# Performance work log

Hardware: AMD Instinct MI355X
Metric: run time of the kernel (lower is better)

The kernel has to match this reference:

```python
import jax, jax.numpy as jnp
import numpy as np

N_ATOMS = 100000
N_EDGES = 200000  # paired: edge 2i and 2i+1 are reverses of each other
N_MOLS = 4096
D_V, D_E, D_H = 133, 14, 512
DEPTH = 3
BN_EPS = 1e-5


def setup_inputs() -> dict:
    key = jax.random.key(0)
    ks = jax.random.split(key, 10)
    V = jax.random.normal(ks[0], (N_ATOMS, D_V), dtype=jnp.float32)
    E = jax.random.normal(ks[1], (N_EDGES, D_E), dtype=jnp.float32)
    # paired directed edges: (src,dst) at 2i, (dst,src) at 2i+1 -> rev index is i^1
    half = N_EDGES // 2
    s = jax.random.randint(ks[2], (half,), 0, N_ATOMS, dtype=jnp.int32)
    d = jax.random.randint(ks[3], (half,), 0, N_ATOMS, dtype=jnp.int32)
    edge_src = jnp.stack([s, d], axis=1).reshape(-1)
    edge_dst = jnp.stack([d, s], axis=1).reshape(-1)
    batch = jnp.sort(jax.random.randint(ks[4], (N_ATOMS,), 0, N_MOLS, dtype=jnp.int32))
    sc = 0.02
    W_i = jax.random.normal(ks[5], (D_V + D_E, D_H), dtype=jnp.float32) * sc
    W_h = jax.random.normal(ks[6], (D_H, D_H), dtype=jnp.float32) * sc
    W_o = jax.random.normal(ks[7], (D_V + D_H, D_H), dtype=jnp.float32) * sc
    b_o = jnp.zeros((D_H,), dtype=jnp.float32)
    gamma = jnp.ones((D_H,), dtype=jnp.float32)
    beta = jnp.zeros((D_H,), dtype=jnp.float32)
    return {"V": V, "E": E, "edge_src": edge_src, "edge_dst": edge_dst,
            "batch": batch, "W_i": W_i, "W_h": W_h, "W_o": W_o, "b_o": b_o,
            "gamma": gamma, "beta": beta}


def reference(V, E, edge_src, edge_dst, batch, W_i, W_h, W_o, b_o, gamma, beta):
    n_atoms = V.shape[0]
    n_edges = E.shape[0]
    rev = jnp.arange(n_edges, dtype=jnp.int32) ^ 1  # reverse-bond index

    # --- BondMessagePassing (chemprop v2) ---
    # initialize: H_0 = W_i([V[src] ; E]), H = relu(H_0)
    H0 = jnp.concatenate([V[edge_src], E], axis=1) @ W_i  # [n_edges, d_h]
    H = jax.nn.relu(H0)
    for _ in range(DEPTH - 1):
        # message: sum of incoming edge states at dst node, gathered at src,
        # minus the reverse edge's own state
        M_node = jax.ops.segment_sum(H, edge_dst, num_segments=n_atoms)
        M = M_node[edge_src] - H[rev]
        # update: H = relu(H_0 + W_h(M)) (dropout = 0)
        H = jax.nn.relu(H0 + M @ W_h)
    # finalize: aggregate edges to nodes, H_v = relu(W_o([V ; M_v]))
    M_v = jax.ops.segment_sum(H, edge_dst, num_segments=n_atoms)
    H_v = jax.nn.relu(jnp.concatenate([V, M_v], axis=1) @ W_o + b_o)  # [n_atoms, d_h]

    # --- MeanAggregation over batch ids ---
    sums = jax.ops.segment_sum(H_v, batch, num_segments=N_MOLS)
    counts = jax.ops.segment_sum(jnp.ones((n_atoms,), H_v.dtype), batch, num_segments=N_MOLS)
    h_mol = sums / jnp.maximum(counts, 1.0)[:, None]  # [n_mols, d_h]

    # --- BatchNorm1d (training mode: batch statistics, biased variance) ---
    mu = h_mol.mean(axis=0)
    var = h_mol.var(axis=0)
    return (h_mol - mu) * jax.lax.rsqrt(var + BN_EPS) * gamma + beta
```

## Files before the change

### kernel.cpp

```cpp
#include <hip/hip_runtime.h>

typedef _Float16 f16;
typedef _Float16 half8 __attribute__((ext_vector_type(8)));
typedef _Float16 half4v __attribute__((ext_vector_type(4)));
typedef float f32x4 __attribute__((ext_vector_type(4)));

#define N_ATOMS 100000
#define N_EDGES 200000
#define N_MOLS  4096
#define D_V 133
#define D_E 14
#define D_H 512
#define KC  672
#define KSE 21
#define LDA 40

__global__ void wt_build_swz(const float* __restrict__ W1, int r1,
                             const float* __restrict__ W2, int r2,
                             f16* __restrict__ WtS) {
    int gid = blockIdx.x * blockDim.x + threadIdx.x;
    if (gid >= D_H * KC) return;
    int n = gid / KC;
    int k = gid - n * KC;
    float x = 0.f;
    if (k < r1) x = W1[k * D_H + n];
    else if (k < r1 + r2) x = W2[(k - r1) * D_H + n];
    const int dst = ((((n >> 4) * KSE + (k >> 5)) << 6) + (((k >> 3) & 3) << 4) + (n & 15)) * 8 + (k & 7);
    WtS[dst] = (f16)x;
}

__global__ void csr_hist(const int* __restrict__ edst, int* __restrict__ cnt) {
    int e = blockIdx.x * blockDim.x + threadIdx.x;
    if (e < N_EDGES) atomicAdd(&cnt[edst[e]], 1);
}

__global__ __launch_bounds__(1024) void csr_scan(const int* __restrict__ cnt,
                                                 int* __restrict__ off, int* __restrict__ pos) {
    __shared__ int sums[1024];
    const int tid = threadIdx.x;
    const int lo = tid * 98;
    const int hi = min(lo + 98, N_ATOMS);
    int s = 0;
    for (int i = lo; i < hi; ++i) s += cnt[i];
    sums[tid] = s;
    __syncthreads();
    for (int d = 1; d < 1024; d <<= 1) {
        int v = (tid >= d) ? sums[tid - d] : 0;
        __syncthreads();
        sums[tid] += v;
        __syncthreads();
    }
    int run = sums[tid] - s;
    for (int i = lo; i < hi; ++i) { off[i] = run; pos[i] = run; run += cnt[i]; }
    if (tid == 1023) off[N_ATOMS] = run;
}

__global__ void csr_scatter(const int* __restrict__ edst, int* __restrict__ pos,
                            int* __restrict__ eid) {
    int e = blockIdx.x * blockDim.x + threadIdx.x;
    if (e < N_EDGES) {
        int idx = atomicAdd(&pos[edst[e]], 1);
        eid[idx] = e;
    }
}

__global__ __launch_bounds__(512) void seg_csr(
    const f16* __restrict__ H, const int* __restrict__ off, const int* __restrict__ eid,
    unsigned int* __restrict__ MnQ32, float* __restrict__ Msc)
{
    const int n = blockIdx.x * 8 + (threadIdx.x >> 6);
    const int lane = threadIdx.x & 63;
    const int j0 = off[n], j1 = off[n + 1];
    float acc[8];
    #pragma unroll
    for (int k = 0; k < 8; ++k) acc[k] = 0.f;
    for (int j = j0; j < j1; ++j) {
        const int e = eid[j];
        const half8 h = *reinterpret_cast<const half8*>(&H[e * D_H + lane * 8]);
        #pragma unroll
        for (int k = 0; k < 8; ++k) acc[k] += (float)h[k];
    }
    float m = 0.f;
    #pragma unroll
    for (int k = 0; k < 8; ++k) m = fmaxf(m, fabsf(acc[k]));
    m = fmaxf(m, __shfl_xor(m, 1));
    m = fmaxf(m, __shfl_xor(m, 2));
    m = fmaxf(m, 1e-20f);
    const float s = m * (1.f / 127.f);
    const float inv_s = 127.f / m;
    if ((lane & 3) == 0) Msc[n * 16 + (lane >> 2)] = s;
    int q[8];
    #pragma unroll
    for (int k = 0; k < 8; ++k) q[k] = __float2int_rn(acc[k] * inv_s);
    uint2 o;
    o.x = (q[0] & 0xff) | ((q[1] & 0xff) << 8) | ((q[2] & 0xff) << 16) | ((unsigned)(q[3] & 0xff) << 24);
    o.y = (q[4] & 0xff) | ((q[5] & 0xff) << 8) | ((q[6] & 0xff) << 16) | ((unsigned)(q[7] & 0xff) << 24);
    *reinterpret_cast<uint2*>(&MnQ32[n * 128 + lane * 2]) = o;
}

__global__ __launch_bounds__(512) void gemm_pass(
    const float* __restrict__ V, const float* __restrict__ E,
    const int* __restrict__ esrc, const char* __restrict__ MnQ,
    const float* __restrict__ Msc,
    f16* __restrict__ Ha, const f16* __restrict__ WtS, int ks_begin)
{
    __shared__ __align__(16) f16 Al[64 * LDA];
    const int tid = threadIdx.x;
    const int rowblk = blockIdx.x << 6;
    const int srow = tid >> 3;
    const int skk  = (tid & 7) << 2;
    const int e_s  = rowblk + srow;
    const int sv   = esrc[e_s];
    const int rev  = e_s ^ 1;
    const int lane = tid & 63;
    const int quad = lane >> 4;
    const int m16  = lane & 15;
    const int colbase = (tid >> 6) << 6;
    const int cb0 = (tid >> 6) << 2;
    const f16* WtL = WtS + lane * 8;

    f32x4 acc[4][4];
    #pragma unroll
    for (int a = 0; a < 4; ++a)
    #pragma unroll
    for (int b = 0; b < 4; ++b)
    #pragma unroll
    for (int r = 0; r < 4; ++r) acc[a][b][r] = 0.f;

    char4 pq; float ps; half4v ph; float pv[4];
    auto issue = [&](int ks) {
        const int k0 = ks << 5;
        if (k0 < D_H) {
            pq = *reinterpret_cast<const char4*>(&MnQ[sv * D_H + k0 + skk]);
            ps = Msc[sv * 16 + (k0 >> 5)];
            ph = *reinterpret_cast<const half4v*>(&Ha[rev * D_H + k0 + skk]);
        } else {
            #pragma unroll
            for (int j = 0; j < 4; ++j) {
                const int kk = k0 + skk + j - D_H;
                float x = 0.f;
                if (kk < D_V) x = V[sv * D_V + kk];
                else if (kk < D_V + D_E) x = E[e_s * D_E + (kk - D_V)];
                pv[j] = x;
            }
        }
    };

    issue(ks_begin);
    for (int ks = ks_begin; ks < KSE; ++ks) {
        const int k0 = ks << 5;
        half4v w;
        if (k0 < D_H) {
            w[0] = (f16)((float)pq.x * ps - (float)ph[0]);
            w[1] = (f16)((float)pq.y * ps - (float)ph[1]);
            w[2] = (f16)((float)pq.z * ps - (float)ph[2]);
            w[3] = (f16)((float)pq.w * ps - (float)ph[3]);
        } else {
            w[0] = (f16)pv[0]; w[1] = (f16)pv[1]; w[2] = (f16)pv[2]; w[3] = (f16)pv[3];
        }
        __syncthreads();
        *reinterpret_cast<half4v*>(&Al[srow * LDA + skk]) = w;
        __syncthreads();
        if (ks + 1 < KSE) issue(ks + 1);
        half8 af[4];
        #pragma unroll
        for (int rt = 0; rt < 4; ++rt)
            af[rt] = *reinterpret_cast<const half8*>(&Al[(rt * 16 + m16) * LDA + quad * 8]);
        #pragma unroll
        for (int ct = 0; ct < 4; ++ct) {
            const half8 bf = *reinterpret_cast<const half8*>(&WtL[(((cb0 + ct) * KSE + ks) << 9)]);
            #pragma unroll
            for (int rt = 0; rt < 4; ++rt)
                acc[rt][ct] = __builtin_amdgcn_mfma_f32_16x16x32_f16(af[rt], bf, acc[rt][ct], 0, 0, 0);
        }
    }

    #pragma unroll
    for (int rt = 0; rt < 4; ++rt)
    #pragma unroll
    for (int ct = 0; ct < 4; ++ct)
    #pragma unroll
    for (int r = 0; r < 4; ++r) {
        const int row = rowblk + rt * 16 + quad * 4 + r;
        const int col = colbase + ct * 16 + m16;
        Ha[row * D_H + col] = (f16)fmaxf(acc[rt][ct][r], 0.f);
    }
}

__global__ __launch_bounds__(512) void gemm_out(
    const float* __restrict__ V, const char* __restrict__ MnQ,
    const float* __restrict__ Msc, const float* __restrict__ bo,
    const f16* __restrict__ WtS, f16* __restrict__ Hv)
{
    __shared__ __align__(16) f16 Al[64 * LDA];
    __shared__ float bo_s[D_H];
    const int tid = threadIdx.x;
    const int rowblk = blockIdx.x << 6;
    bo_s[tid] = bo[tid];
    const int srow = tid >> 3;
    const int skk  = (tid & 7) << 2;
    const int arow = min(rowblk + srow, N_ATOMS - 1);
    const int lane = tid & 63;
    const int quad = lane >> 4;
    const int m16  = lane & 15;
    const int colbase = (tid >> 6) << 6;
    const int cb0 = (tid >> 6) << 2;
    const f16* WtL = WtS + lane * 8;

    f32x4 acc[4][4];
    #pragma unroll
    for (int a = 0; a < 4; ++a)
    #pragma unroll
    for (int b = 0; b < 4; ++b)
    #pragma unroll
    for (int r = 0; r < 4; ++r) acc[a][b][r] = 0.f;

    char4 pq; float ps; float pv[4];
    auto issue = [&](int ks) {
        const int k0 = ks << 5;
        if (k0 < D_H) {
            pq = *reinterpret_cast<const char4*>(&MnQ[arow * D_H + k0 + skk]);
            ps = Msc[arow * 16 + (k0 >> 5)];
        } else {
            #pragma unroll
            for (int j = 0; j < 4; ++j) {
                const int kk = k0 + skk + j - D_H;
                pv[j] = (kk < D_V) ? V[arow * D_V + kk] : 0.f;
            }
        }
    };

    issue(0);
    for (int ks = 0; ks < KSE; ++ks) {
        const int k0 = ks << 5;
        half4v w;
        if (k0 < D_H) {
            w[0] = (f16)((float)pq.x * ps);
            w[1] = (f16)((float)pq.y * ps);
            w[2] = (f16)((float)pq.z * ps);
            w[3] = (f16)((float)pq.w * ps);
        } else {
            w[0] = (f16)pv[0]; w[1] = (f16)pv[1]; w[2] = (f16)pv[2]; w[3] = (f16)pv[3];
        }
        __syncthreads();
        *reinterpret_cast<half4v*>(&Al[srow * LDA + skk]) = w;
        __syncthreads();
        if (ks + 1 < KSE) issue(ks + 1);
        half8 af[4];
        #pragma unroll
        for (int rt = 0; rt < 4; ++rt)
            af[rt] = *reinterpret_cast<const half8*>(&Al[(rt * 16 + m16) * LDA + quad * 8]);
        #pragma unroll
        for (int ct = 0; ct < 4; ++ct) {
            const half8 bf = *reinterpret_cast<const half8*>(&WtL[(((cb0 + ct) * KSE + ks) << 9)]);
            #pragma unroll
            for (int rt = 0; rt < 4; ++rt)
                acc[rt][ct] = __builtin_amdgcn_mfma_f32_16x16x32_f16(af[rt], bf, acc[rt][ct], 0, 0, 0);
        }
    }

    #pragma unroll
    for (int rt = 0; rt < 4; ++rt)
    #pragma unroll
    for (int ct = 0; ct < 4; ++ct)
    #pragma unroll
    for (int r = 0; r < 4; ++r) {
        const int row = rowblk + rt * 16 + quad * 4 + r;
        if (row < N_ATOMS) {
            const int col = colbase + ct * 16 + m16;
            Hv[row * D_H + col] = (f16)fmaxf(acc[rt][ct][r] + bo_s[col], 0.f);
        }
    }
}

__global__ __launch_bounds__(512) void mol_mean(
    const f16* __restrict__ Hv, const int* __restrict__ batch, float* __restrict__ mean)
{
    const int m = blockIdx.x;
    __shared__ int sh[2];
    if (threadIdx.x == 0) {
        int lo = 0, hi = N_ATOMS;
        while (lo < hi) { int mid = (lo + hi) >> 1; if (batch[mid] < m) lo = mid + 1; else hi = mid; }
        sh[0] = lo;
        int lo2 = lo; hi = N_ATOMS;
        while (lo2 < hi) { int mid = (lo2 + hi) >> 1; if (batch[mid] < m + 1) lo2 = mid + 1; else hi = mid; }
        sh[1] = lo2;
    }
    __syncthreads();
    const int a0 = sh[0], a1 = sh[1];
    float acc = 0.f;
    for (int a = a0; a < a1; ++a) acc += (float)Hv[(size_t)a * D_H + threadIdx.x];
    mean[m * D_H + threadIdx.x] = acc / (float)max(a1 - a0, 1);
}

__global__ __launch_bounds__(256) void bn_stats(
    const float* __restrict__ mean_in, const float* __restrict__ gamma,
    const float* __restrict__ beta, float* __restrict__ An, float* __restrict__ Bn)
{
    const int n = blockIdx.x;
    const int tid = threadIdx.x;
    float s = 0.f, s2 = 0.f;
    for (int m = tid; m < N_MOLS; m += 256) {
        float h = mean_in[m * D_H + n];
        s += h; s2 += h * h;
    }
    for (int off = 32; off > 0; off >>= 1) {
        s  += __shfl_down(s, off);
        s2 += __shfl_down(s2, off);
    }
    __shared__ float sh[8];
    const int wave = tid >> 6, lane = tid & 63;
    if (lane == 0) { sh[wave] = s; sh[4 + wave] = s2; }
    __syncthreads();
    if (tid == 0) {
        float S  = sh[0] + sh[1] + sh[2] + sh[3];
        float S2 = sh[4] + sh[5] + sh[6] + sh[7];
        float mu = S / (float)N_MOLS;
        float var = fmaxf(S2 / (float)N_MOLS - mu * mu, 0.f);
        float sc = rsqrtf(var + 1e-5f) * gamma[n];
        An[n] = sc;
        Bn[n] = beta[n] - mu * sc;
    }
}

__global__ void bn_apply(const float* __restrict__ mean_in,
                         const float* __restrict__ An, const float* __restrict__ Bn,
                         float* __restrict__ out)
{
    int gid = blockIdx.x * blockDim.x + threadIdx.x;
    int n = gid & 511;
    out[gid] = mean_in[gid] * An[n] + Bn[n];
}

extern "C" void kernel_launch(void* const* d_in, const int* in_sizes, int n_in,
                              void* d_out, int out_size, void* d_ws, size_t ws_size,
                              hipStream_t stream)
{
    (void)in_sizes; (void)n_in; (void)out_size; (void)ws_size;
    const float* V     = (const float*)d_in[0];
    const float* E     = (const float*)d_in[1];
    const int*   esrc  = (const int*)d_in[2];
    const int*   edst  = (const int*)d_in[3];
    const int*   batch = (const int*)d_in[4];
    const float* Wi    = (const float*)d_in[5];
    const float* Wh    = (const float*)d_in[6];
    const float* Wo    = (const float*)d_in[7];
    const float* bo    = (const float*)d_in[8];
    const float* gam   = (const float*)d_in[9];
    const float* bet   = (const float*)d_in[10];
    float* out = (float*)d_out;

    char* ws = (char*)d_ws;
    f16*   WtC  = (f16*)(ws + 0);
    f16*   WtO  = (f16*)(ws + 688128);
    int*   off  = (int*)(ws + 1376256);
    int*   eid  = (int*)(ws + 1776384);
    int*   cnt  = (int*)(ws + 2576384);
    float* An   = (float*)(ws + 2992768);
    float* Bn   = (float*)(ws + 2994816);
    f16*   Ha   = (f16*)(ws + 2996864);
    char*  MnQ  = (char*)(ws + 207796864);
    float* Msc  = (float*)(ws + 258996864);
    unsigned int* MnQ32 = (unsigned int*)MnQ;
    f16*   Hv   = Ha;
    float* mean = out;

    wt_build_swz<<<(D_H * KC + 255) / 256, 256, 0, stream>>>(Wh, D_H, Wi, D_V + D_E, WtC);
    wt_build_swz<<<(D_H * KC + 255) / 256, 256, 0, stream>>>(Wo + D_V * D_H, D_H, Wo, D_V, WtO);

    hipMemsetAsync(cnt, 0, 400000, stream);
    csr_hist<<<(N_EDGES + 511) / 512, 512, 0, stream>>>(edst, cnt);
    csr_scan<<<1, 1024, 0, stream>>>(cnt, off, cnt);
    csr_scatter<<<(N_EDGES + 511) / 512, 512, 0, stream>>>(edst, cnt, eid);

    gemm_pass<<<N_EDGES / 64, 512, 0, stream>>>(V, E, esrc, MnQ, Msc, Ha, WtC, 16);

    for (int it = 0; it < 2; ++it) {
        seg_csr<<<N_ATOMS / 8, 512, 0, stream>>>(Ha, off, eid, MnQ32, Msc);
        gemm_pass<<<N_EDGES / 64, 512, 0, stream>>>(V, E, esrc, MnQ, Msc, Ha, WtC, 0);
    }

    seg_csr<<<N_ATOMS / 8, 512, 0, stream>>>(Ha, off, eid, MnQ32, Msc);

    gemm_out<<<(N_ATOMS + 63) / 64, 512, 0, stream>>>(V, MnQ, Msc, bo, WtO, Hv);
    mol_mean<<<N_MOLS, 512, 0, stream>>>(Hv, batch, mean);
    bn_stats<<<D_H, 256, 0, stream>>>(mean, gam, bet, An, Bn);
    bn_apply<<<(N_MOLS * D_H) / 256, 256, 0, stream>>>(mean, An, Bn, out);
}
```

Before: 1.516 ms.

## Retile GEMM blocks to 32 rows by 4 waves and dequantize in fp16

Both GEMM kernels move from 64-row tiles with 8 waves to 32-row tiles with 4 waves, each wave covering 128 output columns (2x8 MFMA tiles instead of 4x4). The aim is more blocks, smaller LDS tiles and possibly better occupancy. The cost is that each B fragment from global or L2 is now shared by only 2 row tiles instead of 4, which roughly doubles weight traffic per output. Separately, the int8 message dequantization now runs in packed fp16 arithmetic instead of fp32, trading a little precision for fewer conversion instructions.

```diff
diff --git a/kernel.cpp b/kernel.cpp
--- a/kernel.cpp
+++ b/kernel.cpp
@@ -98,15 +98,15 @@
     *reinterpret_cast<uint2*>(&MnQ32[n * 128 + lane * 2]) = o;
 }
 
-__global__ __launch_bounds__(512) void gemm_pass(
+__global__ __launch_bounds__(256) void gemm_pass(
     const float* __restrict__ V, const float* __restrict__ E,
     const int* __restrict__ esrc, const char* __restrict__ MnQ,
     const float* __restrict__ Msc,
     f16* __restrict__ Ha, const f16* __restrict__ WtS, int ks_begin)
 {
-    __shared__ __align__(16) f16 Al[64 * LDA];
+    __shared__ __align__(16) f16 Al[32 * LDA];
     const int tid = threadIdx.x;
-    const int rowblk = blockIdx.x << 6;
+    const int rowblk = blockIdx.x << 5;
     const int srow = tid >> 3;
     const int skk  = (tid & 7) << 2;
     const int e_s  = rowblk + srow;
@@ -115,24 +115,24 @@
     const int lane = tid & 63;
     const int quad = lane >> 4;
     const int m16  = lane & 15;
-    const int colbase = (tid >> 6) << 6;
-    const int cb0 = (tid >> 6) << 2;
+    const int colbase = (tid >> 6) << 7;
+    const int cb0 = (tid >> 6) << 3;
     const f16* WtL = WtS + lane * 8;
 
-    f32x4 acc[4][4];
-    #pragma unroll
-    for (int a = 0; a < 4; ++a)
-    #pragma unroll
-    for (int b = 0; b < 4; ++b)
+    f32x4 acc[2][8];
+    #pragma unroll
+    for (int a = 0; a < 2; ++a)
+    #pragma unroll
+    for (int b = 0; b < 8; ++b)
     #pragma unroll
     for (int r = 0; r < 4; ++r) acc[a][b][r] = 0.f;
 
-    char4 pq; float ps; half4v ph; float pv[4];
+    char4 pq; f16 psh; half4v ph; float pv[4];
     auto issue = [&](int ks) {
         const int k0 = ks << 5;
         if (k0 < D_H) {
             pq = *reinterpret_cast<const char4*>(&MnQ[sv * D_H + k0 + skk]);
-            ps = Msc[sv * 16 + (k0 >> 5)];
+            psh = (f16)Msc[sv * 16 + (k0 >> 5)];
             ph = *reinterpret_cast<const half4v*>(&Ha[rev * D_H + k0 + skk]);
         } else {
             #pragma unroll
@@ -148,13 +148,15 @@
 
     issue(ks_begin);
     for (int ks = ks_begin; ks < KSE; ++ks) {
-        const int k0 = ks << 5;
         half4v w;
-        if (k0 < D_H) {
-            w[0] = (f16)((float)pq.x * ps - (float)ph[0]);
-            w[1] = (f16)((float)pq.y * ps - (float)ph[1]);
-            w[2] = (f16)((float)pq.z * ps - (float)ph[2]);
-            w[3] = (f16)((float)pq.w * ps - (float)ph[3]);
+        if ((ks << 5) < D_H) {
+            half4v qf;
+            qf[0] = (f16)(short)pq.x; qf[1] = (f16)(short)pq.y;
+            qf[2] = (f16)(short)pq.z; qf[3] = (f16)(short)pq.w;
+            w[0] = qf[0] * psh - ph[0];
+            w[1] = qf[1] * psh - ph[1];
+            w[2] = qf[2] * psh - ph[2];
+            w[3] = qf[3] * psh - ph[3];
         } else {
             w[0] = (f16)pv[0]; w[1] = (f16)pv[1]; w[2] = (f16)pv[2]; w[3] = (f16)pv[3];
         }
@@ -162,23 +164,23 @@
         *reinterpret_cast<half4v*>(&Al[srow * LDA + skk]) = w;
         __syncthreads();
         if (ks + 1 < KSE) issue(ks + 1);
-        half8 af[4];
-        #pragma unroll
-        for (int rt = 0; rt < 4; ++rt)
+        half8 af[2];
+        #pragma unroll
+        for (int rt = 0; rt < 2; ++rt)
             af[rt] = *reinterpret_cast<const half8*>(&Al[(rt * 16 + m16) * LDA + quad * 8]);
         #pragma unroll
-        for (int ct = 0; ct < 4; ++ct) {
+        for (int ct = 0; ct < 8; ++ct) {
             const half8 bf = *reinterpret_cast<const half8*>(&WtL[(((cb0 + ct) * KSE + ks) << 9)]);
             #pragma unroll
-            for (int rt = 0; rt < 4; ++rt)
+            for (int rt = 0; rt < 2; ++rt)
                 acc[rt][ct] = __builtin_amdgcn_mfma_f32_16x16x32_f16(af[rt], bf, acc[rt][ct], 0, 0, 0);
         }
     }
 
     #pragma unroll
-    for (int rt = 0; rt < 4; ++rt)
-    #pragma unroll
-    for (int ct = 0; ct < 4; ++ct)
+    for (int rt = 0; rt < 2; ++rt)
+    #pragma unroll
+    for (int ct = 0; ct < 8; ++ct)
     #pragma unroll
     for (int r = 0; r < 4; ++r) {
         const int row = rowblk + rt * 16 + quad * 4 + r;
@@ -187,40 +189,41 @@
     }
 }
 
-__global__ __launch_bounds__(512) void gemm_out(
+__global__ __launch_bounds__(256) void gemm_out(
     const float* __restrict__ V, const char* __restrict__ MnQ,
     const float* __restrict__ Msc, const float* __restrict__ bo,
     const f16* __restrict__ WtS, f16* __restrict__ Hv)
 {
-    __shared__ __align__(16) f16 Al[64 * LDA];
+    __shared__ __align__(16) f16 Al[32 * LDA];
     __shared__ float bo_s[D_H];
     const int tid = threadIdx.x;
-    const int rowblk = blockIdx.x << 6;
+    const int rowblk = blockIdx.x << 5;
     bo_s[tid] = bo[tid];
+    bo_s[tid + 256] = bo[tid + 256];
     const int srow = tid >> 3;
     const int skk  = (tid & 7) << 2;
     const int arow = min(rowblk + srow, N_ATOMS - 1);
     const int lane = tid & 63;
     const int quad = lane >> 4;
     const int m16  = lane & 15;
-    const int colbase = (tid >> 6) << 6;
-    const int cb0 = (tid >> 6) << 2;
+    const int colbase = (tid >> 6) << 7;
+    const int cb0 = (tid >> 6) << 3;
     const f16* WtL = WtS + lane * 8;
 
-    f32x4 acc[4][4];
-    #pragma unroll
-    for (int a = 0; a < 4; ++a)
-    #pragma unroll
-    for (int b = 0; b < 4; ++b)
+    f32x4 acc[2][8];
+    #pragma unroll
+    for (int a = 0; a < 2; ++a)
+    #pragma unroll
+    for (int b = 0; b < 8; ++b)
     #pragma unroll
     for (int r = 0; r < 4; ++r) acc[a][b][r] = 0.f;
 
-    char4 pq; float ps; float pv[4];
+    char4 pq; f16 psh; float pv[4];
     auto issue = [&](int ks) {
         const int k0 = ks << 5;
         if (k0 < D_H) {
             pq = *reinterpret_cast<const char4*>(&MnQ[arow * D_H + k0 + skk]);
-            ps = Msc[arow * 16 + (k0 >> 5)];
+            psh = (f16)Msc[arow * 16 + (k0 >> 5)];
         } else {
             #pragma unroll
             for (int j = 0; j < 4; ++j) {
@@ -232,13 +235,12 @@
 
     issue(0);
     for (int ks = 0; ks < KSE; ++ks) {
-        const int k0 = ks << 5;
         half4v w;
-        if (k0 < D_H) {
-            w[0] = (f16)((float)pq.x * ps);
-            w[1] = (f16)((float)pq.y * ps);
-            w[2] = (f16)((float)pq.z * ps);
-            w[3] = (f16)((float)pq.w * ps);
+        if ((ks << 5) < D_H) {
+            w[0] = (f16)(short)pq.x * psh;
+            w[1] = (f16)(short)pq.y * psh;
+            w[2] = (f16)(short)pq.z * psh;
+            w[3] = (f16)(short)pq.w * psh;
         } else {
             w[0] = (f16)pv[0]; w[1] = (f16)pv[1]; w[2] = (f16)pv[2]; w[3] = (f16)pv[3];
         }
@@ -246,23 +248,23 @@
         *reinterpret_cast<half4v*>(&Al[srow * LDA + skk]) = w;
         __syncthreads();
         if (ks + 1 < KSE) issue(ks + 1);
-        half8 af[4];
-        #pragma unroll
-        for (int rt = 0; rt < 4; ++rt)
+        half8 af[2];
+        #pragma unroll
+        for (int rt = 0; rt < 2; ++rt)
             af[rt] = *reinterpret_cast<const half8*>(&Al[(rt * 16 + m16) * LDA + quad * 8]);
         #pragma unroll
-        for (int ct = 0; ct < 4; ++ct) {
+        for (int ct = 0; ct < 8; ++ct) {
             const half8 bf = *reinterpret_cast<const half8*>(&WtL[(((cb0 + ct) * KSE + ks) << 9)]);
             #pragma unroll
-            for (int rt = 0; rt < 4; ++rt)
+            for (int rt = 0; rt < 2; ++rt)
                 acc[rt][ct] = __builtin_amdgcn_mfma_f32_16x16x32_f16(af[rt], bf, acc[rt][ct], 0, 0, 0);
         }
     }
 
     #pragma unroll
-    for (int rt = 0; rt < 4; ++rt)
-    #pragma unroll
-    for (int ct = 0; ct < 4; ++ct)
+    for (int rt = 0; rt < 2; ++rt)
+    #pragma unroll
+    for (int ct = 0; ct < 8; ++ct)
     #pragma unroll
     for (int r = 0; r < 4; ++r) {
         const int row = rowblk + rt * 16 + quad * 4 + r;
@@ -373,16 +375,16 @@
     csr_scan<<<1, 1024, 0, stream>>>(cnt, off, cnt);
     csr_scatter<<<(N_EDGES + 511) / 512, 512, 0, stream>>>(edst, cnt, eid);
 
-    gemm_pass<<<N_EDGES / 64, 512, 0, stream>>>(V, E, esrc, MnQ, Msc, Ha, WtC, 16);
+    gemm_pass<<<N_EDGES / 32, 256, 0, stream>>>(V, E, esrc, MnQ, Msc, Ha, WtC, 16);
 
     for (int it = 0; it < 2; ++it) {
         seg_csr<<<N_ATOMS / 8, 512, 0, stream>>>(Ha, off, eid, MnQ32, Msc);
-        gemm_pass<<<N_EDGES / 64, 512, 0, stream>>>(V, E, esrc, MnQ, Msc, Ha, WtC, 0);
+        gemm_pass<<<N_EDGES / 32, 256, 0, stream>>>(V, E, esrc, MnQ, Msc, Ha, WtC, 0);
     }
 
     seg_csr<<<N_ATOMS / 8, 512, 0, stream>>>(Ha, off, eid, MnQ32, Msc);
 
-    gemm_out<<<(N_ATOMS + 63) / 64, 512, 0, stream>>>(V, MnQ, Msc, bo, WtO, Hv);
+    gemm_out<<<N_ATOMS / 32, 256, 0, stream>>>(V, MnQ, Msc, bo, WtO, Hv);
     mol_mean<<<N_MOLS, 512, 0, stream>>>(Hv, batch, mean);
     bn_stats<<<D_H, 256, 0, stream>>>(mean, gam, bet, An, Bn);
     bn_apply<<<(N_MOLS * D_H) / 256, 256, 0, stream>>>(mean, An, Bn, out);
```

Measured after the change: 1.696 ms. 11.9% more time.
